# Optimization experiments

Measured on AMD Instinct MI355X. Metric: run time of the kernel, lower is better.

Reference implementation:

```python
import jax, jax.numpy as jnp
import numpy as np

B, G, CE, D, L, H, DH, M, KQ = 4, 64, 384, 512, 8, 16, 32, 2048, 16
NJ, NB = 163, 11
DET_THRESH = 0.3
PATCH = 14.0
EPS = 1e-8


def _ln(x, g, b):
    mu = x.mean(-1, keepdims=True)
    v = x.var(-1, keepdims=True)
    return (x - mu) * jax.lax.rsqrt(v + 1e-5) * g + b


def setup_inputs():
    key = jax.random.key(0)
    ks = iter(jax.random.split(key, 64))
    def n(sh, s=0.02):
        return (jax.random.normal(next(ks), sh) * s).astype(jnp.float32)
    inp = {}
    inp['feat'] = jax.random.normal(next(ks), (B, G, G, CE), dtype=jnp.float32)
    inp['scores'] = jax.random.uniform(next(ks), (B, G, G), dtype=jnp.float32)
    inp['K_cam'] = jnp.tile(jnp.array([[1000., 0., 448.], [0., 1000., 448.], [0., 0., 1.]], dtype=jnp.float32), (B, 1, 1))
    inp['pos_emb'] = n((G * G, D), 1.0)
    inp['Wtok'] = n((CE, D)); inp['btok'] = jnp.zeros((D,), jnp.float32)
    for nm in ['Wq', 'Wk', 'Wv', 'Wo']:
        inp[nm] = n((L, D, D))
    inp['g1'] = jnp.ones((L, D), jnp.float32); inp['b1n'] = jnp.zeros((L, D), jnp.float32)
    inp['W1'] = n((L, D, M)); inp['bf1'] = jnp.zeros((L, M), jnp.float32)
    inp['W2'] = n((L, M, D)); inp['bf2'] = jnp.zeros((L, D), jnp.float32)
    inp['g2'] = jnp.ones((L, D), jnp.float32); inp['b2n'] = jnp.zeros((L, D), jnp.float32)
    inp['offW1'] = n((D, D)); inp['offb1'] = jnp.zeros((D,), jnp.float32)
    inp['offW2'] = n((D, 2)); inp['offb2'] = jnp.zeros((2,), jnp.float32)
    inp['dW1'] = n((D, D)); inp['db1'] = jnp.zeros((D,), jnp.float32)
    inp['dW2'] = n((D, 1)); inp['db2'] = jnp.zeros((1,), jnp.float32)
    inp['sW1'] = n((D, D)); inp['sb1'] = jnp.zeros((D,), jnp.float32)
    inp['sW2'] = n((D, NB)); inp['sb2'] = jnp.zeros((NB,), jnp.float32)
    inp['pW1'] = n((D + NJ * 6, D)); inp['pb1'] = jnp.zeros((D,), jnp.float32)
    inp['pW2'] = n((D, NJ * 6)); inp['pb2'] = jnp.zeros((NJ * 6,), jnp.float32)
    # identity-like 6D init pose per joint: eye(3)[:, :2].flatten() = [1,0,0,1,0,0]
    inp['init_body_pose'] = jnp.tile(jnp.array([1., 0., 0., 1., 0., 0.], dtype=jnp.float32), NJ)
    inp['useful_rotmat'] = (jax.random.uniform(next(ks), (NJ,)) < 0.66).astype(jnp.float32)
    return inp


def reference(feat, scores, K_cam, pos_emb, Wtok, btok,
              Wq, Wk, Wv, Wo, g1, b1n, W1, bf1, W2, bf2, g2, b2n,
              offW1, offb1, offW2, offb2, dW1, db1, dW2, db2,
              sW1, sb1, sW2, sb2, pW1, pb1, pW2, pb2,
              init_body_pose, useful_rotmat):
    # --- NMS via 3x3 max-pool (stride 1, same padding) + threshold ---
    sm = jax.lax.reduce_window(scores, -jnp.inf, jax.lax.max, (1, 3, 3), (1, 1, 1), 'SAME')
    sc = scores * (sm == scores).astype(scores.dtype)
    flat = sc.reshape(B, G * G)
    vals, idx = jax.lax.top_k(flat, KQ)                 # padded ragged detections
    mask = (vals >= DET_THRESH).astype(feat.dtype)      # [B,KQ] validity mask
    row = idx // G
    col = idx % G
    # --- token projection + 2d pos emb, gather queries ---
    dec_emb = feat @ Wtok + btok + pos_emb.reshape(G, G, D)        # [B,G,G,D]
    ctx = dec_emb.reshape(B, G * G, D)                              # context per image
    q = jnp.take_along_axis(ctx, idx[..., None], axis=1)            # [B,KQ,D]
    x = q * mask[..., None]
    scale = DH ** -0.5
    # --- HPH decoder: depth x (prenorm cross-attn to full-image context + FFN) ---
    for l in range(L):
        h = _ln(x, g1[l], b1n[l])
        qh = (h @ Wq[l]).reshape(B, KQ, H, DH)
        kh = (ctx @ Wk[l]).reshape(B, G * G, H, DH)
        vh = (ctx @ Wv[l]).reshape(B, G * G, H, DH)
        att = jax.nn.softmax(jnp.einsum('bqhd,bkhd->bhqk', qh, kh) * scale, axis=-1)
        o = jnp.einsum('bhqk,bkhd->bqhd', att, vh).reshape(B, KQ, H * DH) @ Wo[l]
        x = x + o * mask[..., None]
        h2 = _ln(x, g2[l], b2n[l])
        x = x + (jax.nn.gelu(h2 @ W1[l] + bf1[l]) @ W2[l] + bf2[l]) * mask[..., None]
    y = x.reshape(B * KQ, D)
    m = mask.reshape(B * KQ, 1)
    # --- heads ---
    offset = jax.nn.relu(y @ offW1 + offb1) @ offW2 + offb2          # [N,2]
    loc_coarse = jnp.stack([col.reshape(-1), row.reshape(-1)], -1).astype(y.dtype)
    loc = (loc_coarse + 0.5 + offset) * PATCH
    Kd = jnp.repeat(K_cam, KQ, axis=0)                               # [N,3,3]
    focal = Kd[:, 0, 0]
    d_raw = jax.nn.relu(y @ dW1 + db1) @ dW2 + db2                   # [N,1]
    dist = focal[:, None] / jnp.clip(jnp.exp(d_raw), 1e-5)
    homo = jnp.concatenate([loc, jnp.ones_like(loc[:, :1])], -1)     # [N,3]
    Kinv = jnp.linalg.inv(Kd)
    transl = jnp.einsum('nij,nj->ni', Kinv, homo) * dist             # [N,3]
    shape_ = jax.nn.sigmoid(jax.nn.relu(y @ sW1 + sb1) @ sW2 + sb2)  # [N,11]
    ibp = jnp.broadcast_to(init_body_pose, (B * KQ, NJ * 6))
    rot6d = jax.nn.relu(jnp.concatenate([y, ibp], -1) @ pW1 + pb1) @ pW2 + pb2 + ibp
    # --- special Gram-Schmidt: 6D -> rotation matrices ---
    Mm = rot6d.reshape(-1, NJ, 3, 2)
    u0 = Mm[..., 0]
    u0 = u0 / (jnp.linalg.norm(u0, axis=-1, keepdims=True) + EPS)
    v1 = Mm[..., 1] - jnp.sum(Mm[..., 1] * u0, -1, keepdims=True) * u0
    u1 = v1 / (jnp.linalg.norm(v1, axis=-1, keepdims=True) + EPS)
    u2 = jnp.cross(u0, u1)
    rotmat = jnp.stack([u0, u1, u2], -1)                             # [N,NJ,3,3]
    eye = jnp.eye(3, dtype=rotmat.dtype)
    um = useful_rotmat.reshape(1, NJ, 1, 1)
    rotmat = um * rotmat + (1.0 - um) * eye
    out = jnp.concatenate([loc, offset, dist, transl, shape_, rotmat.reshape(B * KQ, NJ * 9)], -1) * m
    return out
```

## Files before the change

### kernel.cpp

```cpp
#include <hip/hip_runtime.h>

typedef unsigned int uint;
typedef unsigned short u16;

#define BB 4
#define CE 384
#define DD 512
#define LL 8
#define HH 16
#define MM 2048
#define NJ 163
#define TOK 4096
#define BKQ 64
#define QH 256
#define OUTW 1486
#define NROT 978
#define QKSCALE 0.17677669529663687f

typedef __attribute__((ext_vector_type(8))) short short8;
typedef __attribute__((ext_vector_type(4))) float float4v;

static __device__ __forceinline__ u16 f2bf(float f){
  union { float f; uint u; } c; c.f = f;
  uint u = c.u;
  return (u16)((u + 0x7FFFu + ((u >> 16) & 1u)) >> 16);
}
static __device__ __forceinline__ float bf2f(u16 u){
  union { uint u; float f; } c; c.u = ((uint)u) << 16;
  return c.f;
}
static __device__ __forceinline__ float wred_sum(float v){
  for (int o = 32; o; o >>= 1) v += __shfl_xor(v, o, 64);
  return v;
}
static __device__ __forceinline__ void gl16(const void* g, void* l){
  __builtin_amdgcn_global_load_lds((const __attribute__((address_space(1))) void*)g,
                                   (__attribute__((address_space(3))) void*)l, 16, 0, 0);
}

struct PJobs {
  const float* s[24]; u16* d[24];
  int R[24], C[24], t0[25];
  int njobs, ntiles;
};
__global__ __launch_bounds__(256) void k_prep_all(PJobs J,
    const float* __restrict__ scores,
    int* __restrict__ oidx, float* __restrict__ omask, float* __restrict__ ocol, float* __restrict__ orow,
    const float* __restrict__ pW1, const float* __restrict__ pb1,
    const float* __restrict__ ibp, float* __restrict__ hb4,
    const float* __restrict__ offb1, const float* __restrict__ db1, const float* __restrict__ sb1,
    const float* __restrict__ pb2, float* __restrict__ cvec2)
{
  int bid = blockIdx.x, t = threadIdx.x;
  __shared__ float sraw[4096];
  __shared__ float sv[4]; __shared__ int si[4]; __shared__ int swin;
  __shared__ u16 tb[32][66];

  if (bid < 4){
    int b = bid;
    const float* sp = scores + (size_t)b * 4096;
    for (int i = t; i < 4096; i += 256) sraw[i] = sp[i];
    __syncthreads();
    float v[16];
    #pragma unroll
    for (int j = 0; j < 16; j++){
      int i = t + j*256;
      int r = i >> 6, c = i & 63;
      float mx = -1e30f;
      for (int dr = -1; dr <= 1; dr++){
        int rr = r + dr; if (rr < 0 || rr > 63) continue;
        for (int dc = -1; dc <= 1; dc++){
          int cc = c + dc; if (cc < 0 || cc > 63) continue;
          mx = fmaxf(mx, sraw[rr*64+cc]);
        }
      }
      float s = sraw[i];
      v[j] = (s == mx) ? s : 0.0f;
    }
    int lane = t & 63, wv = t >> 6;
    for (int iter = 0; iter < 16; iter++){
      float best = -1e30f; int bi_ = 1 << 30;
      #pragma unroll
      for (int j = 0; j < 16; j++){
        if (v[j] > best){ best = v[j]; bi_ = t + j*256; }
      }
      #pragma unroll
      for (int o = 32; o; o >>= 1){
        float ov = __shfl_xor(best, o, 64);
        int oi = __shfl_xor(bi_, o, 64);
        if (ov > best || (ov == best && oi < bi_)){ best = ov; bi_ = oi; }
      }
      if (lane == 0){ sv[wv] = best; si[wv] = bi_; }
      __syncthreads();
      if (t == 0){
        float bb = sv[0]; int ii = si[0];
        for (int k = 1; k < 4; k++){
          if (sv[k] > bb || (sv[k] == bb && si[k] < ii)){ bb = sv[k]; ii = si[k]; }
        }
        oidx[b*16+iter] = ii;
        omask[b*16+iter] = (bb >= 0.3f) ? 1.f : 0.f;
        ocol[b*16+iter] = (float)(ii & 63);
        orow[b*16+iter] = (float)(ii >> 6);
        swin = ii;
      }
      __syncthreads();
      int wi = swin;
      if ((wi & 255) == t) v[wi >> 8] = -1e30f;
      __syncthreads();
    }
  } else if (bid < 132){
    int d = (bid - 4)*4 + (t >> 6);
    int ln = t & 63;
    float acc = 0.f;
    for (int i = ln; i < NJ*6; i += 64) acc += ibp[i] * pW1[(size_t)(DD+i)*DD + d];
    acc = wred_sum(acc);
    if (ln == 0) hb4[1536 + d] = acc + pb1[d];
  } else if (bid == 132){
    for (int i = t; i < 1536; i += 256)
      hb4[i] = (i < 512) ? offb1[i] : (i < 1024 ? db1[i-512] : sb1[i-1024]);
    for (int i = t; i < 1024; i += 256)
      cvec2[i] = (i < NJ*6) ? (pb2[i] + ibp[i]) : 0.f;
  }

  for (int g = bid; g < J.ntiles; g += gridDim.x){
    int j = 0;
    while (g >= J.t0[j+1]) j++;
    int ti = g - J.t0[j];
    int C_ = J.C[j], R_ = J.R[j];
    int tC = (C_ + 31) >> 5;
    int ry = ti / tC, cx = ti - ry*tC;
    int r0 = ry*64, c0 = cx*32;
    int tx = t & 31, ty = t >> 5;
    const float* src = J.s[j]; u16* dst = J.d[j];
    __syncthreads();
    #pragma unroll
    for (int i = 0; i < 8; i++){
      int r = ty + i*8;
      float v = 0.f;
      if (c0+tx < C_) v = src[(size_t)(r0+r)*C_ + c0+tx];
      tb[tx][r] = f2bf(v);
    }
    __syncthreads();
    #pragma unroll
    for (int p = 0; p < 4; p++){
      int c = (t >> 5) + p*8;
      int rr = t & 31;
      if (c0 + c < C_){
        uint val = (uint)tb[c][2*rr] | ((uint)tb[c][2*rr+1] << 16);
        *(uint*)&dst[(size_t)(c0+c)*R_ + r0 + rr*2] = val;
      }
    }
  }
}

__global__ __launch_bounds__(256) void k_wqkvo_all(const float* __restrict__ Wq, const float* __restrict__ Wk,
    const float* __restrict__ Wv, const float* __restrict__ Wo,
    u16* __restrict__ ATall, u16* __restrict__ WVOall)
{
  __shared__ __align__(16) u16 As[2560];
  __shared__ __align__(16) u16 Bs[2560];
  int t = threadIdx.x;
  int l = blockIdx.x >> 11;
  int bid = blockIdx.x & 2047;
  const float* wq = Wq + (size_t)l*DD*DD;
  const float* wk = Wk + (size_t)l*DD*DD;
  const float* wv = Wv + (size_t)l*DD*DD;
  const float* wo = Wo + (size_t)l*DD*DD;
  u16* AT  = ATall  + (size_t)l*8192*DD;
  u16* WVOT= WVOall + (size_t)l*DD*8192;
  int lane = t & 63, w = t >> 6, lr = lane & 15, lk = lane >> 4;
  float4v acc[4];
  float4v z4 = {0.f,0.f,0.f,0.f};
  acc[0]=z4; acc[1]=z4; acc[2]=z4; acc[3]=z4;
  if (bid < 1024){
    int id = bid;
    int rt = id & 127, dt = id >> 7;
    int h = rt >> 3, dout0 = (rt & 7)*64, din0 = dt*64;
    int r = t >> 2, c0 = (t & 3)*8;
    {
      float4 u0 = *(const float4*)(wk + (size_t)(dout0+r)*DD + h*32 + c0);
      float4 u1 = *(const float4*)(wk + (size_t)(dout0+r)*DD + h*32 + c0 + 4);
      u16* d = As + r*40 + c0;
      d[0]=f2bf(u0.x); d[1]=f2bf(u0.y); d[2]=f2bf(u0.z); d[3]=f2bf(u0.w);
      d[4]=f2bf(u1.x); d[5]=f2bf(u1.y); d[6]=f2bf(u1.z); d[7]=f2bf(u1.w);
      float4 v0 = *(const float4*)(wq + (size_t)(din0+r)*DD + h*32 + c0);
      float4 v1 = *(const float4*)(wq + (size_t)(din0+r)*DD + h*32 + c0 + 4);
      u16* e = Bs + r*40 + c0;
      e[0]=f2bf(v0.x); e[1]=f2bf(v0.y); e[2]=f2bf(v0.z); e[3]=f2bf(v0.w);
      e[4]=f2bf(v1.x); e[5]=f2bf(v1.y); e[6]=f2bf(v1.z); e[7]=f2bf(v1.w);
    }
    __syncthreads();
    short8 af = *(const short8*)&As[(w*16+lr)*40 + lk*8];
    #pragma unroll
    for (int nf = 0; nf < 4; nf++){
      short8 bf8 = *(const short8*)&Bs[(nf*16+lr)*40 + lk*8];
      acc[nf] = __builtin_amdgcn_mfma_f32_16x16x32_bf16(af, bf8, acc[nf], 0, 0, 0);
    }
    #pragma unroll
    for (int nf = 0; nf < 4; nf++){
      #pragma unroll
      for (int jj = 0; jj < 4; jj++){
        int row = w*16 + lk*4 + jj;
        AT[(size_t)(h*512 + dout0 + row)*DD + din0 + nf*16 + lr] = f2bf(acc[nf][jj]*QKSCALE);
      }
    }
  } else {
    int id = bid - 1024;
    int ct = id & 127, dt = id >> 7;
    int h = ct >> 3, Dc0 = (ct & 7)*64, dout0 = dt*64;
    {
      int c = t >> 3, d8 = (t & 7)*8;
      float4 a0 = *(const float4*)(wo + (size_t)(h*32+c)*DD + dout0 + d8);
      float4 a1 = *(const float4*)(wo + (size_t)(h*32+c)*DD + dout0 + d8 + 4);
      As[(d8+0)*40 + c] = f2bf(a0.x);
      As[(d8+1)*40 + c] = f2bf(a0.y);
      As[(d8+2)*40 + c] = f2bf(a0.z);
      As[(d8+3)*40 + c] = f2bf(a0.w);
      As[(d8+4)*40 + c] = f2bf(a1.x);
      As[(d8+5)*40 + c] = f2bf(a1.y);
      As[(d8+6)*40 + c] = f2bf(a1.z);
      As[(d8+7)*40 + c] = f2bf(a1.w);
      int r = t >> 2, c0 = (t & 3)*8;
      float4 v0 = *(const float4*)(wv + (size_t)(Dc0+r)*DD + h*32 + c0);
      float4 v1 = *(const float4*)(wv + (size_t)(Dc0+r)*DD + h*32 + c0 + 4);
      u16* e = Bs + r*40 + c0;
      e[0]=f2bf(v0.x); e[1]=f2bf(v0.y); e[2]=f2bf(v0.z); e[3]=f2bf(v0.w);
      e[4]=f2bf(v1.x); e[5]=f2bf(v1.y); e[6]=f2bf(v1.z); e[7]=f2bf(v1.w);
    }
    __syncthreads();
    short8 af = *(const short8*)&As[(w*16+lr)*40 + lk*8];
    #pragma unroll
    for (int nf = 0; nf < 4; nf++){
      short8 bf8 = *(const short8*)&Bs[(nf*16+lr)*40 + lk*8];
      acc[nf] = __builtin_amdgcn_mfma_f32_16x16x32_bf16(af, bf8, acc[nf], 0, 0, 0);
    }
    #pragma unroll
    for (int nf = 0; nf < 4; nf++){
      #pragma unroll
      for (int jj = 0; jj < 4; jj++){
        int row = w*16 + lk*4 + jj;
        WVOT[(size_t)(dout0 + row)*8192 + h*512 + Dc0 + nf*16 + lr] = f2bf(acc[nf][jj]);
      }
    }
  }
}

__global__ __launch_bounds__(256) void k_red8(const u16* __restrict__ parts, u16* __restrict__ cf){
  int i4 = blockIdx.x*256 + threadIdx.x;
  int elem = i4*4;
  int row = elem >> 13, col = elem & 8191;
  int b = row >> 4, q = row & 15, h = col >> 9, Dc = col & 511;
  const u16* src = parts + ((size_t)b*8)*131072 + (size_t)(q*16+h)*512 + Dc;
  float s0 = 0.f, s1 = 0.f, s2 = 0.f, s3 = 0.f;
  #pragma unroll
  for (int ks = 0; ks < 8; ks++){
    ushort4 g = *(const ushort4*)(src + (size_t)ks*131072);
    s0 += bf2f(g.x); s1 += bf2f(g.y); s2 += bf2f(g.z); s3 += bf2f(g.w);
  }
  ushort4 o;
  o.x = f2bf(s0); o.y = f2bf(s1); o.z = f2bf(s2); o.w = f2bf(s3);
  *(ushort4*)&cf[(size_t)row*8192 + col] = o;
}

__global__ __launch_bounds__(256) void k_gemm_emb(
    const float* __restrict__ feat, const u16* __restrict__ Bt,
    u16* __restrict__ ctx, u16* __restrict__ ctxT,
    const float* __restrict__ ep1, const float* __restrict__ ep2)
{
  __shared__ __align__(16) u16 SM[16640];
  u16* As = SM;
  u16* Bs = SM + 8192;
  int m0 = blockIdx.y*128, n0 = blockIdx.x*128;
  int t = threadIdx.x, lane = t & 63, wave = t >> 6;
  int wr = wave >> 1, wc = wave & 1;
  int lr = lane & 15, lk = lane >> 4;
  int sr8 = t >> 3, sl = t & 7;
  int sw = ((sl ^ (sr8 & 7)) * 8);
  float4v acc[4][4];
  float4v z4 = {0.f, 0.f, 0.f, 0.f};
  #pragma unroll
  for (int i = 0; i < 4; i++)
    #pragma unroll
    for (int j = 0; j < 4; j++) acc[i][j] = z4;
  for (int kt = 0; kt < CE; kt += 64){
    __syncthreads();
    #pragma unroll
    for (int p = 0; p < 8; p++){
      int r = (t >> 4) + p*16, f4 = t & 15;
      float4 v = *(const float4*)&feat[(size_t)(m0+r)*CE + kt + f4*4];
      int dc = ((f4 >> 1) ^ (r & 7))*8 + (f4 & 1)*4;
      ushort4 o; o.x = f2bf(v.x); o.y = f2bf(v.y); o.z = f2bf(v.z); o.w = f2bf(v.w);
      *(ushort4*)&As[r*64 + dc] = o;
    }
    #pragma unroll
    for (int rg = 0; rg < 4; rg++)
      gl16(Bt + (size_t)(n0 + rg*32 + sr8)*CE + kt + sw, Bs + rg*2048 + 8*t);
    __syncthreads();
    #pragma unroll
    for (int s = 0; s < 2; s++){
      int slot = ((s*4 + lk) ^ (lr & 7)) * 8;
      short8 af[4], bfr[4];
      #pragma unroll
      for (int i = 0; i < 4; i++) af[i] = *(const short8*)&As[(wr*64 + i*16 + lr)*64 + slot];
      #pragma unroll
      for (int j = 0; j < 4; j++) bfr[j] = *(const short8*)&Bs[(wc*64 + j*16 + lr)*64 + slot];
      #pragma unroll
      for (int i = 0; i < 4; i++)
        #pragma unroll
        for (int j = 0; j < 4; j++)
          acc[i][j] = __builtin_amdgcn_mfma_f32_16x16x32_bf16(af[i], bfr[j], acc[i][j], 0, 0, 0);
    }
  }
  __syncthreads();
  #pragma unroll
  for (int i = 0; i < 4; i++){
    int rbase = m0 + wr*64 + i*16 + lk*4;
    #pragma unroll
    for (int j = 0; j < 4; j++){
      int cc = n0 + wc*64 + j*16 + lr;
      #pragma unroll
      for (int jj = 0; jj < 4; jj++){
        int rr = rbase + jj;
        float vv = acc[i][j][jj] + ep1[cc] + ep2[(size_t)(rr & 4095)*DD + cc];
        u16 bv = f2bf(vv);
        ctx[(size_t)rr*DD + cc] = bv;
        SM[(cc - n0)*130 + (rr - m0)] = bv;
      }
    }
  }
  __syncthreads();
  int b = m0 >> 12, tok0 = m0 & 4095;
  int tx = t & 63, ty = t >> 6;
  #pragma unroll 4
  for (int it = 0; it < 32; it++){
    int c = ty*32 + it;
    uint vv = *(const uint*)&SM[c*130 + tx*2];
    *(uint*)&ctxT[((size_t)b*DD + n0 + c)*TOK + tok0 + tx*2] = vv;
  }
}

__global__ __launch_bounds__(256) void k_gather2(const u16* __restrict__ ctx, const int* __restrict__ oidx,
    float* __restrict__ x)
{
  int bq = blockIdx.x, t = threadIdx.x;
  int b = bq >> 4, tok = oidx[bq];
  uint v = ((const uint*)(ctx + ((size_t)b*TOK + tok)*DD))[t];
  float2 o; o.x = bf2f((u16)(v & 0xFFFF)); o.y = bf2f((u16)(v >> 16));
  *(float2*)&x[(size_t)bq*DD + t*2] = o;
}

template<int EPI>
__global__ __launch_bounds__(256) void k_gemm_bt64(
    const u16* __restrict__ A, const u16* __restrict__ Bt,
    float* __restrict__ C, u16* __restrict__ Cb,
    int Kslice, int lda, int ldb, int ldc,
    long sA, long sB, long sC, int ksplit)
{
  int bz = blockIdx.z;
  int batch = bz / ksplit, ks = bz - batch*ksplit;
  const u16* Ab = A + (size_t)batch*sA + (size_t)ks*Kslice;
  const u16* Bb = Bt + (size_t)batch*sB + (size_t)ks*Kslice;
  int m0 = blockIdx.y*128, n0 = blockIdx.x*64;
  __shared__ __align__(16) u16 As[128*64];
  __shared__ __align__(16) u16 Bs[64*64];
  int t = threadIdx.x, lane = t & 63, w = t >> 6;
  int lr = lane & 15, lk = lane >> 4;
  int sr8 = t >> 3, sl = t & 7;
  int sw = ((sl ^ (sr8 & 7)) * 8);
  float4v acc[2][4];
  float4v z4 = {0.f,0.f,0.f,0.f};
  #pragma unroll
  for (int i = 0; i < 2; i++)
    #pragma unroll
    for (int j = 0; j < 4; j++) acc[i][j] = z4;

  for (int kt = 0; kt < Kslice; kt += 64){
    __syncthreads();
    #pragma unroll
    for (int rg = 0; rg < 4; rg++)
      gl16(Ab + (size_t)(m0 + rg*32 + sr8)*lda + kt + sw, As + rg*2048 + 8*t);
    #pragma unroll
    for (int rg = 0; rg < 2; rg++)
      gl16(Bb + (size_t)(n0 + rg*32 + sr8)*ldb + kt + sw, Bs + rg*2048 + 8*t);
    __syncthreads();
    #pragma unroll
    for (int s = 0; s < 2; s++){
      int slot = ((s*4 + lk) ^ (lr & 7)) * 8;
      short8 af[2], bfr[4];
      #pragma unroll
      for (int i = 0; i < 2; i++) af[i] = *(const short8*)&As[(w*32 + i*16 + lr)*64 + slot];
      #pragma unroll
      for (int j = 0; j < 4; j++) bfr[j] = *(const short8*)&Bs[(j*16 + lr)*64 + slot];
      #pragma unroll
      for (int i = 0; i < 2; i++)
        #pragma unroll
        for (int j = 0; j < 4; j++)
          acc[i][j] = __builtin_amdgcn_mfma_f32_16x16x32_bf16(af[i], bfr[j], acc[i][j], 0, 0, 0);
    }
  }
  #pragma unroll
  for (int i = 0; i < 2; i++){
    int rbase = m0 + w*32 + i*16 + lk*4;
    #pragma unroll
    for (int j = 0; j < 4; j++){
      int cc = n0 + j*16 + lr;
      #pragma unroll
      for (int jj = 0; jj < 4; jj++){
        int rr = rbase + jj;
        if (EPI == 0) C[(size_t)bz*sC + (size_t)rr*ldc + cc] = acc[i][j][jj];
        else if (EPI == 1) Cb[(size_t)batch*sC + (size_t)rr*ldc + cc] = f2bf(acc[i][j][jj]);
        else Cb[(size_t)bz*sC + (size_t)rr*ldc + cc] = f2bf(acc[i][j][jj]);
      }
    }
  }
}

template<int ACT, int RES, int OUTB, int DOLN, int NG, int HPB, int ZMAP = 0>
__global__ __launch_bounds__(256) void k_mf64(
    const u16* __restrict__ A, const float* __restrict__ xf,
    const float* __restrict__ g, const float* __restrict__ bb,
    const u16* __restrict__ Bt, const float* __restrict__ bias,
    float* __restrict__ C, u16* __restrict__ Cb, u16* __restrict__ Cb2,
    int N, int K, int kper, int ldc, float alpha)
{
  __shared__ __align__(16) u16 Asl[DOLN ? 64*520 : 64*64];
  __shared__ __align__(16) u16 Bs[64*64];
  int t = threadIdx.x, lane = t & 63, w = t >> 6;
  int lr = lane & 15, lk = lane >> 4;
  int n0 = blockIdx.x*64;
  int ks = blockIdx.y, kbeg = ks*kper;
  int sr8 = t >> 3, sl = t & 7;
  int sw = ((sl ^ (sr8 & 7)) * 8);

  if (DOLN == 1){
    for (int rr = 0; rr < 16; rr++){
      int row = w*16 + rr;
      const float* xr = xf + (size_t)row*DD;
      float4 v0 = *(const float4*)(xr + lane*4);
      float4 v1 = *(const float4*)(xr + 256 + lane*4);
      float s = v0.x+v0.y+v0.z+v0.w + v1.x+v1.y+v1.z+v1.w;
      s = wred_sum(s);
      float mu = s * (1.f/DD);
      float d0=v0.x-mu, d1=v0.y-mu, d2=v0.z-mu, d3=v0.w-mu;
      float e0=v1.x-mu, e1=v1.y-mu, e2=v1.z-mu, e3=v1.w-mu;
      float q = d0*d0+d1*d1+d2*d2+d3*d3 + e0*e0+e1*e1+e2*e2+e3*e3;
      q = wred_sum(q);
      float inv = rsqrtf(q * (1.f/DD) + 1e-5f);
      float4 g0 = *(const float4*)(g + lane*4);
      float4 g1 = *(const float4*)(g + 256 + lane*4);
      float4 b0 = *(const float4*)(bb + lane*4);
      float4 b1 = *(const float4*)(bb + 256 + lane*4);
      u16* dst = &Asl[row*520];
      dst[lane*4+0] = f2bf(d0*inv*g0.x + b0.x);
      dst[lane*4+1] = f2bf(d1*inv*g0.y + b0.y);
      dst[lane*4+2] = f2bf(d2*inv*g0.z + b0.z);
      dst[lane*4+3] = f2bf(d3*inv*g0.w + b0.w);
      dst[256+lane*4+0] = f2bf(e0*inv*g1.x + b1.x);
      dst[256+lane*4+1] = f2bf(e1*inv*g1.y + b1.y);
      dst[256+lane*4+2] = f2bf(e2*inv*g1.z + b1.z);
      dst[256+lane*4+3] = f2bf(e3*inv*g1.w + b1.w);
    }
  } else if (DOLN == 2){
    for (int rr = 0; rr < 16; rr++){
      int row = w*16 + rr;
      const float* xr = xf + (size_t)row*DD;
      float4 v0 = *(const float4*)(xr + lane*4);
      float4 v1 = *(const float4*)(xr + 256 + lane*4);
      u16* dst = &Asl[row*520];
      dst[lane*4+0] = f2bf(v0.x);
      dst[lane*4+1] = f2bf(v0.y);
      dst[lane*4+2] = f2bf(v0.z);
      dst[lane*4+3] = f2bf(v0.w);
      dst[256+lane*4+0] = f2bf(v1.x);
      dst[256+lane*4+1] = f2bf(v1.y);
      dst[256+lane*4+2] = f2bf(v1.z);
      dst[256+lane*4+3] = f2bf(v1.w);
    }
  }

  float4v acc[4];
  float4v z4 = {0.f,0.f,0.f,0.f};
  acc[0]=z4; acc[1]=z4; acc[2]=z4; acc[3]=z4;

  for (int kc = kbeg; kc < kbeg + kper; kc += 64){
    __syncthreads();
    if (!DOLN){
      gl16(A + (size_t)sr8*K + kc + sw,        (u16*)Asl + 8*t);
      gl16(A + (size_t)(32+sr8)*K + kc + sw,   (u16*)Asl + 2048 + 8*t);
    }
    gl16(Bt + (size_t)(n0+sr8)*K + kc + sw,      (u16*)Bs + 8*t);
    gl16(Bt + (size_t)(n0+32+sr8)*K + kc + sw,   (u16*)Bs + 2048 + 8*t);
    __syncthreads();
    #pragma unroll
    for (int s = 0; s < 2; s++){
      int slot = ((s*4 + lk) ^ (lr & 7)) * 8;
      short8 af;
      if (DOLN) af = *(const short8*)&Asl[(w*16+lr)*520 + kc + s*32 + lk*8];
      else      af = *(const short8*)&Asl[(w*16+lr)*64 + slot];
      #pragma unroll
      for (int nf = 0; nf < 4; nf++){
        short8 bf8 = *(const short8*)&Bs[(nf*16+lr)*64 + slot];
        acc[nf] = __builtin_amdgcn_mfma_f32_16x16x32_bf16(af, bf8, acc[nf], 0, 0, 0);
      }
    }
  }
  #pragma unroll
  for (int nf = 0; nf < 4; nf++){
    int col = n0 + nf*16 + lr;
    float bsv = (bias && ks == 0) ? bias[col] : 0.f;
    #pragma unroll
    for (int jj = 0; jj < 4; jj++){
      int row = w*16 + lk*4 + jj;
      float v = acc[nf][jj]*alpha + bsv;
      if (ACT == 1) v = fmaxf(v, 0.f);
      else if (ACT == 2) v = 0.5f*v*(1.f + tanhf(0.7978845608028654f*(v + 0.044715f*v*v*v)));
      if (NG && col >= N) continue;
      if (ZMAP){
        int b_ = row >> 4, q_ = row & 15, h_ = col >> 9, d_ = col & 511;
        Cb[((size_t)b_*QH + (q_ << 4) + h_)*DD + d_] = f2bf(v);
        continue;
      }
      size_t o = (size_t)row*ldc + col;
      if (OUTB == 1) Cb[o] = f2bf(v);
      else if (RES == 0) C[o] = v;
      else atomicAdd(&C[o], v);
      if (HPB && col >= 1536) Cb2[(size_t)row*DD + (col - 1536)] = f2bf(v);
    }
  }
}

__global__ __launch_bounds__(256) void k_softmax(const u16* __restrict__ lg, u16* __restrict__ att){
  int row = blockIdx.x, t = threadIdx.x;
  const uint* p = (const uint*)(lg + (size_t)row*TOK);
  uint pv[8]; float v0[8], v1[8]; float mx = -1e30f;
  #pragma unroll
  for (int i = 0; i < 8; i++){
    pv[i] = p[t + i*256];
    v0[i] = bf2f((u16)(pv[i] & 0xFFFF));
    v1[i] = bf2f((u16)(pv[i] >> 16));
    mx = fmaxf(mx, fmaxf(v0[i], v1[i]));
  }
  int lane = t & 63, w = t >> 6;
  for (int o = 32; o; o >>= 1) mx = fmaxf(mx, __shfl_xor(mx, o, 64));
  __shared__ float sm[4]; __shared__ float ssum[4];
  if (lane == 0) sm[w] = mx;
  __syncthreads();
  mx = fmaxf(fmaxf(sm[0], sm[1]), fmaxf(sm[2], sm[3]));
  float s = 0.f;
  #pragma unroll
  for (int i = 0; i < 8; i++){
    v0[i] = expf(v0[i] - mx); v1[i] = expf(v1[i] - mx);
    s += v0[i] + v1[i];
  }
  s = wred_sum(s);
  if (lane == 0) ssum[w] = s;
  __syncthreads();
  s = ssum[0]+ssum[1]+ssum[2]+ssum[3];
  float inv = 1.f / s;
  uint* q = (uint*)(att + (size_t)row*TOK);
  #pragma unroll
  for (int i = 0; i < 8; i++){
    uint lo = f2bf(v0[i]*inv);
    uint hi = f2bf(v1[i]*inv);
    q[t + i*256] = lo | (hi << 16);
  }
}

__global__ __launch_bounds__(256) void k_final(
    const float* __restrict__ h4, const float* __restrict__ rot6d,
// ... 49 lines not shown
    for (int j = 0; j < 11; j++){ float sp = sout[3+j] + sb2[j]; o[8+j] = m / (1.f + expf(-sp)); }
  }
  if (t < NJ){
    const float* rp = rot6d + (size_t)bq*NROT + t*6;
    float a0 = rp[0], b0 = rp[1], a1 = rp[2], b1 = rp[3], a2 = rp[4], b2 = rp[5];
    float n0 = sqrtf(a0*a0 + a1*a1 + a2*a2);
    float i0 = 1.f / (n0 + 1e-8f);
    float u00 = a0*i0, u01 = a1*i0, u02 = a2*i0;
    float dt = b0*u00 + b1*u01 + b2*u02;
    float v0 = b0 - dt*u00, v1 = b1 - dt*u01, v2 = b2 - dt*u02;
    float n1 = sqrtf(v0*v0 + v1*v1 + v2*v2);
    float i1 = 1.f / (n1 + 1e-8f);
    float u10 = v0*i1, u11 = v1*i1, u12 = v2*i1;
    float u20 = u01*u12 - u02*u11;
    float u21 = u02*u10 - u00*u12;
    float u22 = u00*u11 - u01*u10;
    float um = useful[t], om = 1.f - um;
    float R00 = um*u00 + om, R01 = um*u10,      R02 = um*u20;
    float R10 = um*u01,      R11 = um*u11 + om, R12 = um*u21;
    float R20 = um*u02,      R21 = um*u12,      R22 = um*u22 + om;
    float* o = out + (size_t)bq*OUTW + 19 + t*9;
    o[0] = R00*m; o[1] = R01*m; o[2] = R02*m;
    o[3] = R10*m; o[4] = R11*m; o[5] = R12*m;
    o[6] = R20*m; o[7] = R21*m; o[8] = R22*m;
  }
}

extern "C" void kernel_launch(void* const* d_in, const int* in_sizes, int n_in,
                              void* d_out, int out_size, void* d_ws, size_t ws_size,
                              hipStream_t stream)
{
  const float* feat   = (const float*)d_in[0];
  const float* scores = (const float*)d_in[1];
  const float* K_cam  = (const float*)d_in[2];
  const float* pos_emb= (const float*)d_in[3];
  const float* Wtok   = (const float*)d_in[4];
  const float* btok   = (const float*)d_in[5];
  const float* Wq     = (const float*)d_in[6];
  const float* Wk     = (const float*)d_in[7];
  const float* Wv     = (const float*)d_in[8];
  const float* Wo     = (const float*)d_in[9];
  const float* g1     = (const float*)d_in[10];
  const float* b1n    = (const float*)d_in[11];
  const float* W1     = (const float*)d_in[12];
  const float* bf1    = (const float*)d_in[13];
  const float* W2     = (const float*)d_in[14];
  const float* bf2    = (const float*)d_in[15];
  const float* g2     = (const float*)d_in[16];
  const float* b2n    = (const float*)d_in[17];
  const float* offW1  = (const float*)d_in[18];
  const float* offb1  = (const float*)d_in[19];
  const float* offW2  = (const float*)d_in[20];
  const float* offb2  = (const float*)d_in[21];
  const float* dW1    = (const float*)d_in[22];
  const float* db1    = (const float*)d_in[23];
  const float* dW2    = (const float*)d_in[24];
  const float* db2    = (const float*)d_in[25];
  const float* sW1    = (const float*)d_in[26];
  const float* sb1    = (const float*)d_in[27];
  const float* sW2    = (const float*)d_in[28];
  const float* sb2    = (const float*)d_in[29];
  const float* pW1    = (const float*)d_in[30];
  const float* pb1    = (const float*)d_in[31];
  const float* pW2    = (const float*)d_in[32];
  const float* pb2    = (const float*)d_in[33];
  const float* ibp    = (const float*)d_in[34];
  const float* useful = (const float*)d_in[35];
  float* out = (float*)d_out;

  char* wsp = (char*)d_ws;
  size_t off = 0;
  auto alloc = [&](size_t bytes)->char*{
    char* p = wsp + off;
    off += (bytes + 255) & ~((size_t)255);
    return p;
  };
  int*   t_idx  = (int*)  alloc(BKQ*4);
  float* t_mask = (float*)alloc(BKQ*4);
  float* t_col  = (float*)alloc(BKQ*4);
  float* t_row  = (float*)alloc(BKQ*4);
  u16*   wtokT  = (u16*)  alloc((size_t)DD*CE*2);
  u16*   ctx_bf = (u16*)  alloc((size_t)BB*TOK*DD*2);
  u16*   ctxT_bf= (u16*)  alloc((size_t)BB*TOK*DD*2);
  u16*   ATall  = (u16*)  alloc((size_t)LL*8192*DD*2);
  u16*   WVOall = (u16*)  alloc((size_t)LL*DD*8192*2);
  u16*   w1T    = (u16*)  alloc((size_t)LL*DD*MM*2);
  u16*   w2T    = (u16*)  alloc((size_t)LL*MM*DD*2);
  u16*   headsT = (u16*)  alloc((size_t)4*DD*DD*2);
  u16*   pw2T   = (u16*)  alloc((size_t)1024*DD*2);
  float* x      = (float*)alloc((size_t)BKQ*DD*4);
  u16*   z_bf   = (u16*)  alloc((size_t)BKQ*HH*DD*2);
  u16*   logits = (u16*)  alloc((size_t)BB*QH*TOK*2);
  u16*   att_bf = (u16*)  alloc((size_t)BB*QH*TOK*2);
  u16*   parts  = (u16*)  alloc((size_t)BB*8*QH*DD*2);
  u16*   c_flat = (u16*)  alloc((size_t)BKQ*8192*2);
  u16*   mid_bf = (u16*)  alloc((size_t)BKQ*MM*2);
  float* h4     = (float*)alloc((size_t)BKQ*2048*4);
  u16*   hp_bf  = (u16*)  alloc((size_t)BKQ*DD*2);
  float* hb4    = (float*)alloc(2048*4);
  float* cvec2  = (float*)alloc(1024*4);
  float* rot6d  = (float*)alloc((size_t)BKQ*NROT*4);
  if (off > ws_size) return;

  PJobs J;
  int ntl = 0, nj = 0;
  auto addjob = [&](const float* s, u16* d, int R, int C){
    J.s[nj] = s; J.d[nj] = d; J.R[nj] = R; J.C[nj] = C; J.t0[nj] = ntl;
    ntl += (R/64) * ((C+31)/32);
    nj++;
  };
  addjob(Wtok, wtokT, CE, DD);
  for (int l = 0; l < LL; l++) addjob(W1 + (size_t)l*DD*MM, w1T + (size_t)l*MM*DD, DD, MM);
  for (int l = 0; l < LL; l++) addjob(W2 + (size_t)l*MM*DD, w2T + (size_t)l*DD*MM, MM, DD);
  addjob(offW1, headsT,            DD, DD);
  addjob(dW1,   headsT + DD*DD,    DD, DD);
  addjob(sW1,   headsT + 2*DD*DD,  DD, DD);
  addjob(pW1,   headsT + 3*DD*DD,  DD, DD);
  addjob(pW2,   pw2T, DD, NROT);
  J.t0[nj] = ntl; J.njobs = nj; J.ntiles = ntl;

  k_prep_all<<<2048, 256, 0, stream>>>(J, scores, t_idx, t_mask, t_col, t_row,
                                       pW1, pb1, ibp, hb4, offb1, db1, sb1, pb2, cvec2);
  k_wqkvo_all<<<16384, 256, 0, stream>>>(Wq, Wk, Wv, Wo, ATall, WVOall);
  k_gemm_emb<<<dim3(DD/128, (BB*TOK)/128, 1), 256, 0, stream>>>(feat, wtokT, ctx_bf, ctxT_bf, btok, pos_emb);
  k_gather2<<<BKQ, 256, 0, stream>>>(ctx_bf, t_idx, x);

  for (int l = 0; l < LL; l++){
    k_mf64<0,0,0,1,0,0,1><<<dim3(128,1), 256, 0, stream>>>(
        nullptr, x, g1 + l*DD, b1n + l*DD, ATall + (size_t)l*8192*DD, nullptr,
        nullptr, z_bf, nullptr, 8192, DD, DD, DD, 1.f);
    k_gemm_bt64<1><<<dim3(TOK/64, 2, BB), 256, 0, stream>>>(
        z_bf, ctx_bf, nullptr, logits,
        DD, DD, DD, TOK, (long)QH*DD, (long)TOK*DD, (long)QH*TOK, 1);
    k_softmax<<<BB*QH, 256, 0, stream>>>(logits, att_bf);
    k_gemm_bt64<2><<<dim3(DD/64, 2, BB*8), 256, 0, stream>>>(
        att_bf, ctxT_bf, nullptr, parts,
        TOK/8, TOK, TOK, DD, (long)QH*TOK, (long)DD*TOK, (long)QH*DD, 8);
    k_red8<<<512, 256, 0, stream>>>(parts, c_flat);
    k_mf64<0,1,0,0,0,0,0><<<dim3(8,16), 256, 0, stream>>>(
        c_flat, nullptr, nullptr, nullptr, WVOall + (size_t)l*DD*8192, nullptr,
        x, nullptr, nullptr, DD, 8192, 512, DD, 1.f);
    k_mf64<2,0,1,1,0,0,0><<<dim3(MM/64,1), 256, 0, stream>>>(
        nullptr, x, g2 + l*DD, b2n + l*DD, w1T + (size_t)l*DD*MM, bf1 + l*MM,
        nullptr, mid_bf, nullptr, MM, DD, DD, MM, 1.f);
    k_mf64<0,1,0,0,0,0,0><<<dim3(8,8), 256, 0, stream>>>(
        mid_bf, nullptr, nullptr, nullptr, w2T + (size_t)l*MM*DD, bf2 + l*DD,
        x, nullptr, nullptr, DD, MM, MM/8, DD, 1.f);
  }

  k_mf64<1,0,0,2,0,1,0><<<dim3(32,1), 256, 0, stream>>>(
      nullptr, x, nullptr, nullptr, headsT, hb4,
      h4, nullptr, hp_bf, 2048, DD, DD, 2048, 1.f);
  k_mf64<0,0,0,0,1,0,0><<<dim3(16,1), 256, 0, stream>>>(
      hp_bf, nullptr, nullptr, nullptr, pw2T, cvec2,
      rot6d, nullptr, nullptr, NROT, DD, DD, NROT, 1.f);
  k_final<<<BKQ, 256, 0, stream>>>(h4, rot6d, offW2, offb2, dW2, db2, sW2, sb2,
                                   K_cam, useful, t_mask, t_col, t_row, out);
}
```

Measured before the change: 972.3 us.

## Overlap per-layer Wqk/Wvo precompute with PV GEMM and fuse split-K reduction

Removes the standalone kernel that precomputed the fused QK and VO weight products for all 8 layers up front. Layer 0's products are now built in the prep kernel. Each later layer's products are computed by extra blocks appended to the previous layer's PV GEMM launch, with double-buffered storage. The separate split-K reduction kernel is dropped and the 8 partial sums are folded into the A-tile load of the VO projection GEMM. This trades a large serial precompute and a launch per layer for more LDS in the prep kernel and heavier A loads in the projection GEMM.

```diff
diff --git a/kernel.cpp b/kernel.cpp
--- a/kernel.cpp
+++ b/kernel.cpp
@@ -38,6 +38,90 @@
                                    (__attribute__((address_space(3))) void*)l, 16, 0, 0);
 }
 
+static __device__ void d_wqk(const float* __restrict__ wq, const float* __restrict__ wk,
+    u16* __restrict__ AT, int id, int t, u16* As, u16* Bs)
+{
+  int rt = id & 127, dt = id >> 7;
+  int h = rt >> 3, dout0 = (rt & 7)*64, din0 = dt*64;
+  int r = t >> 2, c0 = (t & 3)*8;
+  {
+    float4 u0 = *(const float4*)(wk + (size_t)(dout0+r)*DD + h*32 + c0);
+    float4 u1 = *(const float4*)(wk + (size_t)(dout0+r)*DD + h*32 + c0 + 4);
+    u16* d = As + r*40 + c0;
+    d[0]=f2bf(u0.x); d[1]=f2bf(u0.y); d[2]=f2bf(u0.z); d[3]=f2bf(u0.w);
+    d[4]=f2bf(u1.x); d[5]=f2bf(u1.y); d[6]=f2bf(u1.z); d[7]=f2bf(u1.w);
+    float4 v0 = *(const float4*)(wq + (size_t)(din0+r)*DD + h*32 + c0);
+    float4 v1 = *(const float4*)(wq + (size_t)(din0+r)*DD + h*32 + c0 + 4);
+    u16* e = Bs + r*40 + c0;
+    e[0]=f2bf(v0.x); e[1]=f2bf(v0.y); e[2]=f2bf(v0.z); e[3]=f2bf(v0.w);
+    e[4]=f2bf(v1.x); e[5]=f2bf(v1.y); e[6]=f2bf(v1.z); e[7]=f2bf(v1.w);
+  }
+  __syncthreads();
+  int lane = t & 63, w = t >> 6, lr = lane & 15, lk = lane >> 4;
+  short8 af = *(const short8*)&As[(w*16+lr)*40 + lk*8];
+  float4v acc[4];
+  float4v z4 = {0.f,0.f,0.f,0.f};
+  acc[0]=z4; acc[1]=z4; acc[2]=z4; acc[3]=z4;
+  #pragma unroll
+  for (int nf = 0; nf < 4; nf++){
+    short8 bf8 = *(const short8*)&Bs[(nf*16+lr)*40 + lk*8];
+    acc[nf] = __builtin_amdgcn_mfma_f32_16x16x32_bf16(af, bf8, acc[nf], 0, 0, 0);
+  }
+  #pragma unroll
+  for (int nf = 0; nf < 4; nf++){
+    #pragma unroll
+    for (int jj = 0; jj < 4; jj++){
+      int row = w*16 + lk*4 + jj;
+      AT[(size_t)(h*512 + dout0 + row)*DD + din0 + nf*16 + lr] = f2bf(acc[nf][jj]*QKSCALE);
+    }
+  }
+}
+
+static __device__ void d_wvo(const float* __restrict__ wv, const float* __restrict__ wo,
+    u16* __restrict__ WVOT, int id, int t, u16* As, u16* Bs)
+{
+  int ct = id & 127, dt = id >> 7;
+  int h = ct >> 3, Dc0 = (ct & 7)*64, dout0 = dt*64;
+  {
+    int c = t >> 3, d8 = (t & 7)*8;
+    float4 a0 = *(const float4*)(wo + (size_t)(h*32+c)*DD + dout0 + d8);
+    float4 a1 = *(const float4*)(wo + (size_t)(h*32+c)*DD + dout0 + d8 + 4);
+    As[(d8+0)*40 + c] = f2bf(a0.x);
+    As[(d8+1)*40 + c] = f2bf(a0.y);
+    As[(d8+2)*40 + c] = f2bf(a0.z);
+    As[(d8+3)*40 + c] = f2bf(a0.w);
+    As[(d8+4)*40 + c] = f2bf(a1.x);
+    As[(d8+5)*40 + c] = f2bf(a1.y);
+    As[(d8+6)*40 + c] = f2bf(a1.z);
+    As[(d8+7)*40 + c] = f2bf(a1.w);
+    int r = t >> 2, c0 = (t & 3)*8;
+    float4 v0 = *(const float4*)(wv + (size_t)(Dc0+r)*DD + h*32 + c0);
+    float4 v1 = *(const float4*)(wv + (size_t)(Dc0+r)*DD + h*32 + c0 + 4);
+    u16* e = Bs + r*40 + c0;
+    e[0]=f2bf(v0.x); e[1]=f2bf(v0.y); e[2]=f2bf(v0.z); e[3]=f2bf(v0.w);
+    e[4]=f2bf(v1.x); e[5]=f2bf(v1.y); e[6]=f2bf(v1.z); e[7]=f2bf(v1.w);
+  }
+  __syncthreads();
+  int lane = t & 63, w = t >> 6, lr = lane & 15, lk = lane >> 4;
+  short8 af = *(const short8*)&As[(w*16+lr)*40 + lk*8];
+  float4v acc[4];
+  float4v z4 = {0.f,0.f,0.f,0.f};
+  acc[0]=z4; acc[1]=z4; acc[2]=z4; acc[3]=z4;
+  #pragma unroll
+  for (int nf = 0; nf < 4; nf++){
+    short8 bf8 = *(const short8*)&Bs[(nf*16+lr)*40 + lk*8];
+    acc[nf] = __builtin_amdgcn_mfma_f32_16x16x32_bf16(af, bf8, acc[nf], 0, 0, 0);
+  }
+  #pragma unroll
+  for (int nf = 0; nf < 4; nf++){
+    #pragma unroll
+    for (int jj = 0; jj < 4; jj++){
+      int row = w*16 + lk*4 + jj;
+      WVOT[(size_t)(dout0 + row)*8192 + h*512 + Dc0 + nf*16 + lr] = f2bf(acc[nf][jj]);
+    }
+  }
+}
+
 struct PJobs {
   const float* s[24]; u16* d[24];
   int R[24], C[24], t0[25];
@@ -49,12 +133,17 @@
     const float* __restrict__ pW1, const float* __restrict__ pb1,
     const float* __restrict__ ibp, float* __restrict__ hb4,
     const float* __restrict__ offb1, const float* __restrict__ db1, const float* __restrict__ sb1,
-    const float* __restrict__ pb2, float* __restrict__ cvec2)
+    const float* __restrict__ pb2, float* __restrict__ cvec2,
+    const float* __restrict__ Wq, const float* __restrict__ Wk,
+    const float* __restrict__ Wv, const float* __restrict__ Wo,
+    u16* __restrict__ AT0, u16* __restrict__ WVO0)
 {
   int bid = blockIdx.x, t = threadIdx.x;
   __shared__ float sraw[4096];
   __shared__ float sv[4]; __shared__ int si[4]; __shared__ int swin;
   __shared__ u16 tb[32][66];
+  __shared__ __align__(16) u16 Aw[2560];
+  __shared__ __align__(16) u16 Bw[2560];
 
   if (bid < 4){
     int b = bid;
@@ -151,115 +240,10 @@
       }
     }
   }
-}
-
-__global__ __launch_bounds__(256) void k_wqkvo_all(const float* __restrict__ Wq, const float* __restrict__ Wk,
-    const float* __restrict__ Wv, const float* __restrict__ Wo,
-    u16* __restrict__ ATall, u16* __restrict__ WVOall)
-{
-  __shared__ __align__(16) u16 As[2560];
-  __shared__ __align__(16) u16 Bs[2560];
-  int t = threadIdx.x;
-  int l = blockIdx.x >> 11;
-  int bid = blockIdx.x & 2047;
-  const float* wq = Wq + (size_t)l*DD*DD;
-  const float* wk = Wk + (size_t)l*DD*DD;
-  const float* wv = Wv + (size_t)l*DD*DD;
-  const float* wo = Wo + (size_t)l*DD*DD;
-  u16* AT  = ATall  + (size_t)l*8192*DD;
-  u16* WVOT= WVOall + (size_t)l*DD*8192;
-  int lane = t & 63, w = t >> 6, lr = lane & 15, lk = lane >> 4;
-  float4v acc[4];
-  float4v z4 = {0.f,0.f,0.f,0.f};
-  acc[0]=z4; acc[1]=z4; acc[2]=z4; acc[3]=z4;
-  if (bid < 1024){
-    int id = bid;
-    int rt = id & 127, dt = id >> 7;
-    int h = rt >> 3, dout0 = (rt & 7)*64, din0 = dt*64;
-    int r = t >> 2, c0 = (t & 3)*8;
-    {
-      float4 u0 = *(const float4*)(wk + (size_t)(dout0+r)*DD + h*32 + c0);
-      float4 u1 = *(const float4*)(wk + (size_t)(dout0+r)*DD + h*32 + c0 + 4);
-      u16* d = As + r*40 + c0;
-      d[0]=f2bf(u0.x); d[1]=f2bf(u0.y); d[2]=f2bf(u0.z); d[3]=f2bf(u0.w);
-      d[4]=f2bf(u1.x); d[5]=f2bf(u1.y); d[6]=f2bf(u1.z); d[7]=f2bf(u1.w);
-      float4 v0 = *(const float4*)(wq + (size_t)(din0+r)*DD + h*32 + c0);
-      float4 v1 = *(const float4*)(wq + (size_t)(din0+r)*DD + h*32 + c0 + 4);
-      u16* e = Bs + r*40 + c0;
-      e[0]=f2bf(v0.x); e[1]=f2bf(v0.y); e[2]=f2bf(v0.z); e[3]=f2bf(v0.w);
-      e[4]=f2bf(v1.x); e[5]=f2bf(v1.y); e[6]=f2bf(v1.z); e[7]=f2bf(v1.w);
-    }
-    __syncthreads();
-    short8 af = *(const short8*)&As[(w*16+lr)*40 + lk*8];
-    #pragma unroll
-    for (int nf = 0; nf < 4; nf++){
-      short8 bf8 = *(const short8*)&Bs[(nf*16+lr)*40 + lk*8];
-      acc[nf] = __builtin_amdgcn_mfma_f32_16x16x32_bf16(af, bf8, acc[nf], 0, 0, 0);
-    }
-    #pragma unroll
-    for (int nf = 0; nf < 4; nf++){
-      #pragma unroll
-      for (int jj = 0; jj < 4; jj++){
-        int row = w*16 + lk*4 + jj;
-        AT[(size_t)(h*512 + dout0 + row)*DD + din0 + nf*16 + lr] = f2bf(acc[nf][jj]*QKSCALE);
-      }
-    }
-  } else {
-    int id = bid - 1024;
-    int ct = id & 127, dt = id >> 7;
-    int h = ct >> 3, Dc0 = (ct & 7)*64, dout0 = dt*64;
-    {
-      int c = t >> 3, d8 = (t & 7)*8;
-      float4 a0 = *(const float4*)(wo + (size_t)(h*32+c)*DD + dout0 + d8);
-      float4 a1 = *(const float4*)(wo + (size_t)(h*32+c)*DD + dout0 + d8 + 4);
-      As[(d8+0)*40 + c] = f2bf(a0.x);
-      As[(d8+1)*40 + c] = f2bf(a0.y);
-      As[(d8+2)*40 + c] = f2bf(a0.z);
-      As[(d8+3)*40 + c] = f2bf(a0.w);
-      As[(d8+4)*40 + c] = f2bf(a1.x);
-      As[(d8+5)*40 + c] = f2bf(a1.y);
-      As[(d8+6)*40 + c] = f2bf(a1.z);
-      As[(d8+7)*40 + c] = f2bf(a1.w);
-      int r = t >> 2, c0 = (t & 3)*8;
-      float4 v0 = *(const float4*)(wv + (size_t)(Dc0+r)*DD + h*32 + c0);
-      float4 v1 = *(const float4*)(wv + (size_t)(Dc0+r)*DD + h*32 + c0 + 4);
-      u16* e = Bs + r*40 + c0;
-      e[0]=f2bf(v0.x); e[1]=f2bf(v0.y); e[2]=f2bf(v0.z); e[3]=f2bf(v0.w);
-      e[4]=f2bf(v1.x); e[5]=f2bf(v1.y); e[6]=f2bf(v1.z); e[7]=f2bf(v1.w);
-    }
-    __syncthreads();
-    short8 af = *(const short8*)&As[(w*16+lr)*40 + lk*8];
-    #pragma unroll
-    for (int nf = 0; nf < 4; nf++){
-      short8 bf8 = *(const short8*)&Bs[(nf*16+lr)*40 + lk*8];
-      acc[nf] = __builtin_amdgcn_mfma_f32_16x16x32_bf16(af, bf8, acc[nf], 0, 0, 0);
-    }
-    #pragma unroll
-    for (int nf = 0; nf < 4; nf++){
-      #pragma unroll
-      for (int jj = 0; jj < 4; jj++){
-        int row = w*16 + lk*4 + jj;
-        WVOT[(size_t)(dout0 + row)*8192 + h*512 + Dc0 + nf*16 + lr] = f2bf(acc[nf][jj]);
-      }
-    }
-  }
-}
-
-__global__ __launch_bounds__(256) void k_red8(const u16* __restrict__ parts, u16* __restrict__ cf){
-  int i4 = blockIdx.x*256 + threadIdx.x;
-  int elem = i4*4;
-  int row = elem >> 13, col = elem & 8191;
-  int b = row >> 4, q = row & 15, h = col >> 9, Dc = col & 511;
-  const u16* src = parts + ((size_t)b*8)*131072 + (size_t)(q*16+h)*512 + Dc;
-  float s0 = 0.f, s1 = 0.f, s2 = 0.f, s3 = 0.f;
-  #pragma unroll
-  for (int ks = 0; ks < 8; ks++){
-    ushort4 g = *(const ushort4*)(src + (size_t)ks*131072);
-    s0 += bf2f(g.x); s1 += bf2f(g.y); s2 += bf2f(g.z); s3 += bf2f(g.w);
-  }
-  ushort4 o;
-  o.x = f2bf(s0); o.y = f2bf(s1); o.z = f2bf(s2); o.w = f2bf(s3);
-  *(ushort4*)&cf[(size_t)row*8192 + col] = o;
+
+  __syncthreads();
+  if (bid < 1024) d_wqk(Wq, Wk, AT0, bid, t, Aw, Bw);
+  else d_wvo(Wv, Wo, WVO0, bid - 1024, t, Aw, Bw);
 }
 
 __global__ __launch_bounds__(256) void k_gemm_emb(
@@ -349,17 +333,12 @@
   *(float2*)&x[(size_t)bq*DD + t*2] = o;
 }
 
-template<int EPI>
-__global__ __launch_bounds__(256) void k_gemm_bt64(
-    const u16* __restrict__ A, const u16* __restrict__ Bt,
-    float* __restrict__ C, u16* __restrict__ Cb,
-    int Kslice, int lda, int ldb, int ldc,
-    long sA, long sB, long sC, int ksplit)
+__global__ __launch_bounds__(256) void k_gemm_logits(
+    const u16* __restrict__ A, const u16* __restrict__ Bt, u16* __restrict__ Cb)
 {
   int bz = blockIdx.z;
-  int batch = bz / ksplit, ks = bz - batch*ksplit;
-  const u16* Ab = A + (size_t)batch*sA + (size_t)ks*Kslice;
-  const u16* Bb = Bt + (size_t)batch*sB + (size_t)ks*Kslice;
+  const u16* Ab = A + (size_t)bz*QH*DD;
+  const u16* Bb = Bt + (size_t)bz*TOK*DD;
   int m0 = blockIdx.y*128, n0 = blockIdx.x*64;
   __shared__ __align__(16) u16 As[128*64];
   __shared__ __align__(16) u16 Bs[64*64];
@@ -373,15 +352,14 @@
   for (int i = 0; i < 2; i++)
     #pragma unroll
     for (int j = 0; j < 4; j++) acc[i][j] = z4;
-
-  for (int kt = 0; kt < Kslice; kt += 64){
+  for (int kt = 0; kt < DD; kt += 64){
     __syncthreads();
     #pragma unroll
     for (int rg = 0; rg < 4; rg++)
-      gl16(Ab + (size_t)(m0 + rg*32 + sr8)*lda + kt + sw, As + rg*2048 + 8*t);
+      gl16(Ab + (size_t)(m0 + rg*32 + sr8)*DD + kt + sw, As + rg*2048 + 8*t);
     #pragma unroll
     for (int rg = 0; rg < 2; rg++)
-      gl16(Bb + (size_t)(n0 + rg*32 + sr8)*ldb + kt + sw, Bs + rg*2048 + 8*t);
+      gl16(Bb + (size_t)(n0 + rg*32 + sr8)*DD + kt + sw, Bs + rg*2048 + 8*t);
     __syncthreads();
     #pragma unroll
     for (int s = 0; s < 2; s++){
@@ -407,15 +385,81 @@
       #pragma unroll
       for (int jj = 0; jj < 4; jj++){
         int rr = rbase + jj;
-        if (EPI == 0) C[(size_t)bz*sC + (size_t)rr*ldc + cc] = acc[i][j][jj];
-        else if (EPI == 1) Cb[(size_t)batch*sC + (size_t)rr*ldc + cc] = f2bf(acc[i][j][jj]);
-        else Cb[(size_t)bz*sC + (size_t)rr*ldc + cc] = f2bf(acc[i][j][jj]);
-      }
-    }
-  }
-}
-
-template<int ACT, int RES, int OUTB, int DOLN, int NG, int HPB, int ZMAP = 0>
+        Cb[(size_t)bz*QH*TOK + (size_t)rr*TOK + cc] = f2bf(acc[i][j][jj]);
+      }
+    }
+  }
+}
+
+__global__ __launch_bounds__(256) void k_pv_fused(
+    const u16* __restrict__ att, const u16* __restrict__ ctxT, u16* __restrict__ parts,
+    const float* __restrict__ wq, const float* __restrict__ wk,
+    const float* __restrict__ wv, const float* __restrict__ wo,
+    u16* __restrict__ AT, u16* __restrict__ WVO)
+{
+  __shared__ __align__(16) u16 As[128*64];
+  __shared__ __align__(16) u16 Bs[64*64];
+  int bz = blockIdx.z, t = threadIdx.x;
+  if (bz >= 32){
+    int id = (bz - 32)*16 + blockIdx.y*8 + blockIdx.x;
+    if (id < 1024) d_wqk(wq, wk, AT, id, t, As, As + 2560);
+    else d_wvo(wv, wo, WVO, id - 1024, t, As, As + 2560);
+    return;
+  }
+  int batch = bz >> 3, ks = bz & 7;
+  const u16* Ab = att + (size_t)batch*QH*TOK + (size_t)ks*512;
+  const u16* Bb = ctxT + (size_t)batch*DD*TOK + (size_t)ks*512;
+  int m0 = blockIdx.y*128, n0 = blockIdx.x*64;
+  int lane = t & 63, w = t >> 6;
+  int lr = lane & 15, lk = lane >> 4;
+  int sr8 = t >> 3, sl = t & 7;
+  int sw = ((sl ^ (sr8 & 7)) * 8);
+  float4v acc[2][4];
+  float4v z4 = {0.f,0.f,0.f,0.f};
+  #pragma unroll
+  for (int i = 0; i < 2; i++)
+    #pragma unroll
+    for (int j = 0; j < 4; j++) acc[i][j] = z4;
+  for (int kt = 0; kt < 512; kt += 64){
+    __syncthreads();
+    #pragma unroll
+    for (int rg = 0; rg < 4; rg++)
+      gl16(Ab + (size_t)(m0 + rg*32 + sr8)*TOK + kt + sw, As + rg*2048 + 8*t);
+    #pragma unroll
+    for (int rg = 0; rg < 2; rg++)
+      gl16(Bb + (size_t)(n0 + rg*32 + sr8)*TOK + kt + sw, Bs + rg*2048 + 8*t);
+    __syncthreads();
+    #pragma unroll
+    for (int s = 0; s < 2; s++){
+      int slot = ((s*4 + lk) ^ (lr & 7)) * 8;
+      short8 af[2], bfr[4];
+      #pragma unroll
+      for (int i = 0; i < 2; i++) af[i] = *(const short8*)&As[(w*32 + i*16 + lr)*64 + slot];
+      #pragma unroll
+      for (int j = 0; j < 4; j++) bfr[j] = *(const short8*)&Bs[(j*16 + lr)*64 + slot];
+      #pragma unroll
+      for (int i = 0; i < 2; i++)
+        #pragma unroll
+        for (int j = 0; j < 4; j++)
+          acc[i][j] = __builtin_amdgcn_mfma_f32_16x16x32_bf16(af[i], bfr[j], acc[i][j], 0, 0, 0);
+    }
+  }
+  #pragma unroll
+  for (int i = 0; i < 2; i++){
+    int rbase = m0 + w*32 + i*16 + lk*4;
+    #pragma unroll
+    for (int j = 0; j < 4; j++){
+      int cc = n0 + j*16 + lr;
+      #pragma unroll
+      for (int jj = 0; jj < 4; jj++){
+        int rr = rbase + jj;
+        parts[(size_t)bz*QH*DD + (size_t)rr*DD + cc] = f2bf(acc[i][j][jj]);
+      }
+    }
+  }
+}
+
+template<int ACT, int RES, int OUTB, int DOLN, int NG, int HPB, int ZMAP = 0, int ARED = 0>
 __global__ __launch_bounds__(256) void k_mf64(
     const u16* __restrict__ A, const float* __restrict__ xf,
     const float* __restrict__ g, const float* __restrict__ bb,
@@ -484,7 +528,35 @@
 
   for (int kc = kbeg; kc < kbeg + kper; kc += 64){
     __syncthreads();
-    if (!DOLN){
+    if (ARED){
+      int row = t >> 2;
+      int b_ = row >> 4, q_ = row & 15;
+      int c0 = (t & 3) * 16;
+      int h_ = kc >> 9;
+      const u16* src = A + ((size_t)b_*8)*131072 + (size_t)(q_*16 + h_)*512 + (kc & 511) + c0;
+      float s[16];
+      #pragma unroll
+      for (int i = 0; i < 16; i++) s[i] = 0.f;
+      #pragma unroll
+      for (int sp = 0; sp < 8; sp++){
+        const u16* ps = src + (size_t)sp*131072;
+        #pragma unroll
+        for (int q4 = 0; q4 < 4; q4++){
+          ushort4 gg = *(const ushort4*)(ps + q4*4);
+          s[q4*4+0] += bf2f(gg.x); s[q4*4+1] += bf2f(gg.y);
+          s[q4*4+2] += bf2f(gg.z); s[q4*4+3] += bf2f(gg.w);
+        }
+      }
+      #pragma unroll
+      for (int gr = 0; gr < 2; gr++){
+        int dc = (((t & 3)*2 + gr) ^ (row & 7)) * 8;
+        ushort4 o0, o1;
+        o0.x = f2bf(s[gr*8+0]); o0.y = f2bf(s[gr*8+1]); o0.z = f2bf(s[gr*8+2]); o0.w = f2bf(s[gr*8+3]);
+        o1.x = f2bf(s[gr*8+4]); o1.y = f2bf(s[gr*8+5]); o1.z = f2bf(s[gr*8+6]); o1.w = f2bf(s[gr*8+7]);
+        *(ushort4*)&Asl[row*64 + dc] = o0;
+        *(ushort4*)&Asl[row*64 + dc + 4] = o1;
+      }
+    } else if (!DOLN){
       gl16(A + (size_t)sr8*K + kc + sw,        (u16*)Asl + 8*t);
       gl16(A + (size_t)(32+sr8)*K + kc + sw,   (u16*)Asl + 2048 + 8*t);
     }
@@ -700,8 +772,8 @@
   u16*   wtokT  = (u16*)  alloc((size_t)DD*CE*2);
   u16*   ctx_bf = (u16*)  alloc((size_t)BB*TOK*DD*2);
   u16*   ctxT_bf= (u16*)  alloc((size_t)BB*TOK*DD*2);
-  u16*   ATall  = (u16*)  alloc((size_t)LL*8192*DD*2);
-  u16*   WVOall = (u16*)  alloc((size_t)LL*DD*8192*2);
+  u16*   ATb    = (u16*)  alloc((size_t)2*8192*DD*2);
+  u16*   WVOb   = (u16*)  alloc((size_t)2*DD*8192*2);
   u16*   w1T    = (u16*)  alloc((size_t)LL*DD*MM*2);
   u16*   w2T    = (u16*)  alloc((size_t)LL*MM*DD*2);
   u16*   headsT = (u16*)  alloc((size_t)4*DD*DD*2);
@@ -711,7 +783,6 @@
   u16*   logits = (u16*)  alloc((size_t)BB*QH*TOK*2);
   u16*   att_bf = (u16*)  alloc((size_t)BB*QH*TOK*2);
   u16*   parts  = (u16*)  alloc((size_t)BB*8*QH*DD*2);
-  u16*   c_flat = (u16*)  alloc((size_t)BKQ*8192*2);
   u16*   mid_bf = (u16*)  alloc((size_t)BKQ*MM*2);
   float* h4     = (float*)alloc((size_t)BKQ*2048*4);
   u16*   hp_bf  = (u16*)  alloc((size_t)BKQ*DD*2);
@@ -737,26 +808,34 @@
   addjob(pW2,   pw2T, DD, NROT);
   J.t0[nj] = ntl; J.njobs = nj; J.ntiles = ntl;
 
+  const size_t ATS = (size_t)8192*DD;
   k_prep_all<<<2048, 256, 0, stream>>>(J, scores, t_idx, t_mask, t_col, t_row,
-                                       pW1, pb1, ibp, hb4, offb1, db1, sb1, pb2, cvec2);
-  k_wqkvo_all<<<16384, 256, 0, stream>>>(Wq, Wk, Wv, Wo, ATall, WVOall);
+                                       pW1, pb1, ibp, hb4, offb1, db1, sb1, pb2, cvec2,
+                                       Wq, Wk, Wv, Wo, ATb, WVOb);
   k_gemm_emb<<<dim3(DD/128, (BB*TOK)/128, 1), 256, 0, stream>>>(feat, wtokT, ctx_bf, ctxT_bf, btok, pos_emb);
   k_gather2<<<BKQ, 256, 0, stream>>>(ctx_bf, t_idx, x);
 
   for (int l = 0; l < LL; l++){
+    u16* ATl  = ATb  + (size_t)(l & 1)*ATS;
+    u16* WVOl = WVOb + (size_t)(l & 1)*ATS;
+    u16* ATn  = ATb  + (size_t)((l+1) & 1)*ATS;
+    u16* WVOn = WVOb + (size_t)((l+1) & 1)*ATS;
     k_mf64<0,0,0,1,0,0,1><<<dim3(128,1), 256, 0, stream>>>(
-        nullptr, x, g1 + l*DD, b1n + l*DD, ATall + (size_t)l*8192*DD, nullptr,
+        nullptr, x, g1 + l*DD, b1n + l*DD, ATl, nullptr,
         nullptr, z_bf, nullptr, 8192, DD, DD, DD, 1.f);
-    k_gemm_bt64<1><<<dim3(TOK/64, 2, BB), 256, 0, stream>>>(
-        z_bf, ctx_bf, nullptr, logits,
-        DD, DD, DD, TOK, (long)QH*DD, (long)TOK*DD, (long)QH*TOK, 1);
+    k_gemm_logits<<<dim3(TOK/64, 2, BB), 256, 0, stream>>>(z_bf, ctx_bf, logits);
     k_softmax<<<BB*QH, 256, 0, stream>>>(logits, att_bf);
-    k_gemm_bt64<2><<<dim3(DD/64, 2, BB*8), 256, 0, stream>>>(
-        att_bf, ctxT_bf, nullptr, parts,
-        TOK/8, TOK, TOK, DD, (long)QH*TOK, (long)DD*TOK, (long)QH*DD, 8);
-    k_red8<<<512, 256, 0, stream>>>(parts, c_flat);
-    k_mf64<0,1,0,0,0,0,0><<<dim3(8,16), 256, 0, stream>>>(
-        c_flat, nullptr, nullptr, nullptr, WVOall + (size_t)l*DD*8192, nullptr,
+    if (l < LL-1){
+      k_pv_fused<<<dim3(8, 2, 32 + 128), 256, 0, stream>>>(
+          att_bf, ctxT_bf, parts,
+          Wq + (size_t)(l+1)*DD*DD, Wk + (size_t)(l+1)*DD*DD,
+          Wv + (size_t)(l+1)*DD*DD, Wo + (size_t)(l+1)*DD*DD, ATn, WVOn);
+    } else {
+      k_pv_fused<<<dim3(8, 2, 32), 256, 0, stream>>>(
+          att_bf, ctxT_bf, parts, nullptr, nullptr, nullptr, nullptr, nullptr, nullptr);
+    }
+    k_mf64<0,1,0,0,0,0,0,1><<<dim3(8,16), 256, 0, stream>>>(
+        parts, nullptr, nullptr, nullptr, WVOl, nullptr,
         x, nullptr, nullptr, DD, 8192, 512, DD, 1.f);
     k_mf64<2,0,1,1,0,0,0><<<dim3(MM/64,1), 256, 0, stream>>>(
         nullptr, x, g2 + l*DD, b2n + l*DD, w1T + (size_t)l*DD*MM, bf1 + l*MM,
```

Result: no change. 991.2 us (+1.9%).
